# Kernel optimization log

Hardware: AMD Instinct MI355X
Metric: run time of the kernel (lower is better)

## Reference

```python
import jax, jax.numpy as jnp
import numpy as np

B, N = 16, 2048
NOTE, BEAT_H, MEAS_H, FINAL_H = 512, 128, 64, 128
NUM_BEATS, NUM_MEAS = 256, 64
OUT = 11            # output_size; QPM_INDEX = 0
QPM = 0


def _uniform(k, shape, fan):
    b = 1.0 / np.sqrt(fan)
    return jax.random.uniform(k, shape, jnp.float32, -b, b)


def _lstm_cell(x, h, c, wih, whh, bih, bhh):
    g = x @ wih.T + bih + h @ whh.T + bhh
    ii, ff, gg, oo = jnp.split(g, 4, axis=-1)
    c2 = jax.nn.sigmoid(ff) * c + jax.nn.sigmoid(ii) * jnp.tanh(gg)
    return jax.nn.sigmoid(oo) * jnp.tanh(c2), c2


def setup_inputs() -> dict:
    key = jax.random.key(0)
    ks = jax.random.split(key, 20)
    note_emb = jax.random.normal(ks[0], (B, N, NOTE), jnp.float32)
    beat_emb = jax.random.normal(ks[1], (B, NUM_BEATS, BEAT_H), jnp.float32)
    measure_emb = jax.random.normal(ks[2], (B, NUM_MEAS, MEAS_H), jnp.float32)
    beat_numbers = jnp.sort(jax.random.randint(ks[3], (B, N), 0, NUM_BEATS), axis=1)
    measure_numbers = beat_numbers // (NUM_BEATS // NUM_MEAS)
    tin = BEAT_H + MEAS_H + 1 + (OUT - 1)   # beat-tempo LSTM input size
    fin = NOTE + BEAT_H + MEAS_H + OUT      # final LSTM input size
    d = OUT - 1
    return {
        "note_emb": note_emb, "beat_emb": beat_emb, "measure_emb": measure_emb,
        "beat_numbers": beat_numbers, "measure_numbers": measure_numbers,
        "Wa": _uniform(ks[4], (d, d), d), "ba": _uniform(ks[5], (d,), d),
        "ctx": _uniform(ks[6], (d,), d),
        "Wih_t": _uniform(ks[7], (4 * BEAT_H, tin), BEAT_H),
        "Whh_t": _uniform(ks[8], (4 * BEAT_H, BEAT_H), BEAT_H),
        "bih_t": _uniform(ks[9], (4 * BEAT_H,), BEAT_H),
        "bhh_t": _uniform(ks[10], (4 * BEAT_H,), BEAT_H),
        "Wih_f": _uniform(ks[11], (4 * FINAL_H, fin), FINAL_H),
        "Whh_f": _uniform(ks[12], (4 * FINAL_H, FINAL_H), FINAL_H),
        "bih_f": _uniform(ks[13], (4 * FINAL_H,), FINAL_H),
        "bhh_f": _uniform(ks[14], (4 * FINAL_H,), FINAL_H),
        "W_fc": _uniform(ks[15], (d, FINAL_H), FINAL_H),
        "b_fc": _uniform(ks[16], (d,), FINAL_H),
        "W_tfc": _uniform(ks[17], (1, BEAT_H), BEAT_H),
        "b_tfc": _uniform(ks[18], (1,), BEAT_H),
    }


def _decode(note_emb, beat_emb, measure_emb, beat_numbers, measure_numbers,
            Wa, ba, ctx, Wih_t, Whh_t, bih_t, bhh_t,
            Wih_f, Whh_f, bih_f, bhh_f, W_fc, b_fc, W_tfc, b_tfc):
    Bn, Nn = note_emb.shape[0], note_emb.shape[1]
    d = W_fc.shape[0]  # OUT - 1
    zs_beat = jnp.maximum(beat_numbers - beat_numbers[:, :1], 0)
    zs_meas = jnp.maximum(measure_numbers - measure_numbers[:, :1], 0)
    diff = jnp.diff(beat_numbers, axis=1)
    # beat_changed: first step forced to 1, then diff of beat numbers
    changed_all = jnp.concatenate([jnp.ones((Bn, 1), diff.dtype), diff], axis=1) > 0
    pos = jnp.arange(Nn)
    bidx = jnp.arange(Bn)

    carry0 = (
        jnp.zeros((Bn, BEAT_H)), jnp.zeros((Bn, BEAT_H)),        # tempo h, c
        jnp.zeros((Bn, FINAL_H)), jnp.zeros((Bn, FINAL_H)),      # final h, c
        jnp.zeros((Bn, d + 1)),                                   # prev_out
        jnp.zeros((Bn, beat_emb.shape[1], d)),                    # beat_results
        jnp.zeros((Bn, Nn, d + 1)),                               # out_total
    )

    def step(carry, i):
        th, tc, fh, fc_, prev_out, beat_results, out_total = carry
        changed = changed_all[:, i]                                # [B] bool
        # --- get_beat_corresp_out: notes j < i in the beat just finished ---
        prev_beat = beat_numbers[:, jnp.maximum(i - 1, 0)]         # [B]
        note_mask = (beat_numbers == prev_beat[:, None]) & (pos[None, :] < i)
        x = out_total[:, :, QPM + 1:]                              # [B,N,d]
        sim = (x @ Wa.T + ba) @ ctx                                # [B,N]
        sim = jnp.where(note_mask, sim, -1e9)
        w = jax.nn.softmax(sim, axis=1)
        result_node = jnp.einsum('bn,bnd->bd', w, x)
        result_node = jnp.where(note_mask.any(axis=1)[:, None], result_node, 0.0)
        cb = zs_beat[:, i]
        cm = zs_meas[:, i]
        # scatter result_node into beat_results only for batches whose beat changed
        old = beat_results[bidx, cb]
        beat_results = beat_results.at[bidx, cb].set(
            jnp.where(changed[:, None], result_node, old))
        # --- beat tempo RNN step (only applied where changed) ---
        tempo_in = jnp.concatenate([
            beat_emb[bidx, cb], measure_emb[bidx, cm],
            prev_out[:, QPM:QPM + 1], beat_results[bidx, cb]], axis=-1)
        th2, tc2 = _lstm_cell(tempo_in, th, tc, Wih_t, Whh_t, bih_t, bhh_t)
        th = jnp.where(changed[:, None], th2, th)
        tc = jnp.where(changed[:, None], tc2, tc)
        tmp_tempo = th2 @ W_tfc.T + b_tfc                          # [B,1]
        prev_out = prev_out.at[:, QPM:QPM + 1].set(
            jnp.where(changed[:, None], tmp_tempo, prev_out[:, QPM:QPM + 1]))
        # --- final note-level LSTM step (all batches) ---
        fin_in = jnp.concatenate([
            note_emb[:, i], beat_emb[bidx, cb], measure_emb[bidx, cm], prev_out], axis=-1)
        fh, fc_ = _lstm_cell(fin_in, fh, fc_, Wih_f, Whh_f, bih_f, bhh_f)
        out = fh @ W_fc.T + b_fc                                   # [B,d]
        prev_out = jnp.concatenate([prev_out[:, :QPM + 1], out], axis=-1)
        out_total = out_total.at[:, i].set(prev_out)
        return (th, tc, fh, fc_, prev_out, beat_results, out_total), None

    carry, _ = jax.lax.scan(step, carry0, jnp.arange(Nn))
    out_total = carry[-1]
    # zero out padded notes (note embedding all-zero rows)
    pad = (note_emb.sum(-1) == 0)[:, :, None]
    return jnp.where(pad, 0.0, out_total)


def reference(note_emb, beat_emb, measure_emb, beat_numbers, measure_numbers,
              Wa, ba, ctx, Wih_t, Whh_t, bih_t, bhh_t,
              Wih_f, Whh_f, bih_f, bhh_f, W_fc, b_fc, W_tfc, b_tfc):
    return _decode(note_emb, beat_emb, measure_emb, beat_numbers, measure_numbers,
                   Wa, ba, ctx, Wih_t, Whh_t, bih_t, bhh_t,
                   Wih_f, Whh_f, bih_f, bhh_f, W_fc, b_fc, W_tfc, b_tfc)
```

## Files before the change

kernel.cpp:

```cpp
#include <hip/hip_runtime.h>
#include <cstdint>
#include <cstddef>

#define B_      16
#define N_      2048
#define NOTE_   512
#define BEAT_H_ 128
#define MEAS_H_ 64
#define NBEATS_ 256
#define NMEAS_  64
#define OUT_    11
#define D_      10
#define TSTRIDE 136

typedef float f32x4 __attribute__((ext_vector_type(4)));
typedef unsigned int u32x4 __attribute__((ext_vector_type(4)));
typedef _Float16 h2v __attribute__((ext_vector_type(2)));

__device__ __forceinline__ float fexp2_(float x) {
#if __has_builtin(__builtin_amdgcn_exp2f)
    return __builtin_amdgcn_exp2f(x);
#else
    return exp2f(x);
#endif
}
__device__ __forceinline__ float frcp_(float x) {
#if __has_builtin(__builtin_amdgcn_rcpf)
    return __builtin_amdgcn_rcpf(x);
#else
    return 1.0f / x;
#endif
}
__device__ __forceinline__ float sigm_(float x) {
    return frcp_(1.0f + fexp2_(-1.4426950408889634f * x));
}
__device__ __forceinline__ float tanh_(float x) {
    return 1.0f - 2.0f * frcp_(fexp2_(2.8853900817779268f * x) + 1.0f);
}

__device__ __forceinline__ float dot2f_(unsigned wu, unsigned hu, float c) {
    union { unsigned u; h2v h; } a, bb;
    a.u = wu; bb.u = hu;
#if __has_builtin(__builtin_amdgcn_fdot2)
    return __builtin_amdgcn_fdot2(a.h, bb.h, c, false);
#else
    return c + (float)a.h[0] * (float)bb.h[0] + (float)a.h[1] * (float)bb.h[1];
#endif
}

__device__ __align__(16) _Float16 g_whh_h16[512 * 128];
__device__ float g_bias_eff[512];
__device__ float g_wtail0[512];
__device__ __align__(16) _Float16 g_wht_h16[512 * TSTRIDE];

__global__ __launch_bounds__(256) void pad_k(const float* __restrict__ note,
                                             int* __restrict__ padf) {
    int wave = threadIdx.x >> 6, lane = threadIdx.x & 63;
    int r = blockIdx.x * 4 + wave;
    const float* row = note + ((size_t)r << 9);
    float s = 0.f;
#pragma unroll
    for (int u = 0; u < 8; ++u) s += row[lane + (u << 6)];
#pragma unroll
    for (int off = 32; off; off >>= 1) s += __shfl_xor(s, off, 64);
    if (lane == 0) padf[r] = (s == 0.0f) ? 1 : 0;
}

__global__ __launch_bounds__(128) void fold_whh(
    const float* __restrict__ Whh_f, const float* __restrict__ Wih_f,
    const float* __restrict__ W_fc, const float* __restrict__ b_fc) {
    int gr = blockIdx.x;
    int t = threadIdx.x;
    __shared__ float tail[OUT_];
    if (t < OUT_) tail[t] = Wih_f[(size_t)gr * 715 + 704 + t];
    __syncthreads();
    float m = Whh_f[(size_t)gr * 128 + t];
#pragma unroll
    for (int d = 0; d < D_; ++d) m += tail[1 + d] * W_fc[d * 128 + t];
    g_whh_h16[(size_t)gr * 128 + t] = (_Float16)m;
    if (t == 0) {
        float bb = 0.f;
#pragma unroll
        for (int d = 0; d < D_; ++d) bb += tail[1 + d] * b_fc[d];
        g_bias_eff[gr] = bb;
        g_wtail0[gr] = tail[0];
    }
}

__global__ __launch_bounds__(128) void fold_wht(const float* __restrict__ Whh_t) {
    int gr = blockIdx.x, t = threadIdx.x;
    g_wht_h16[(size_t)gr * TSTRIDE + t] = (_Float16)Whh_t[(size_t)gr * 128 + t];
    if (t < TSTRIDE - 128) g_wht_h16[(size_t)gr * TSTRIDE + 128 + t] = (_Float16)0.f;
}

__global__ __launch_bounds__(256) void tempo_pre_k(
    const float* __restrict__ beat, const float* __restrict__ meas,
    const int* __restrict__ bnum, const int* __restrict__ mnum,
    const float* __restrict__ Wih_t, const float* __restrict__ bih_t,
    const float* __restrict__ bhh_t, float* __restrict__ tpre) {
    __shared__ float sin_[16][192];
    int b = blockIdx.x, qt = blockIdx.y;
    int t = threadIdx.x;
    int bn0 = bnum[b << 11], mn0 = mnum[b << 11];
    for (int idx = t; idx < 16 * 192; idx += 256) {
        int qq = idx / 192, kk = idx - qq * 192;
        int q = qt * 16 + qq;
        float v;
        if (kk < 128) {
            v = beat[(size_t)(b * NBEATS_ + q) * 128 + kk];
        } else {
            int cm = ((q + bn0) >> 2) - mn0;
            if (cm > 63) cm = 63;
            if (cm < 0) cm = 0;
            v = meas[(size_t)(b * NMEAS_ + cm) * 64 + (kk - 128)];
        }
        sin_[qq][kk] = v;
    }
    __syncthreads();
    for (int half = 0; half < 2; ++half) {
        int j = t + half * 256;
        const float* wr = Wih_t + (size_t)j * 203;
        float bias = bih_t[j] + bhh_t[j];
        float acc[16] = {};
        for (int k = 0; k < 192; ++k) {
            float w = wr[k];
#pragma unroll
            for (int qq = 0; qq < 16; ++qq) acc[qq] += w * sin_[qq][k];
        }
        for (int qq = 0; qq < 16; ++qq)
            tpre[(size_t)(b * NBEATS_ + qt * 16 + qq) * 512 + j] = acc[qq] + bias;
    }
}

__global__ __launch_bounds__(256) void fin_pre_gemm(
    const float* __restrict__ note, const float* __restrict__ beat,
    const float* __restrict__ meas, const int* __restrict__ bnum,
    const int* __restrict__ mnum, const float* __restrict__ Wih_f,
    const float* __restrict__ bih_f, const float* __restrict__ bhh_f,
    float* __restrict__ finp) {
    __shared__ float As[16][64];
    __shared__ float Bs[16][64];
    int t = threadIdx.x;
    int r0 = blockIdx.x * 64;
    int j0 = blockIdx.y * 64;

    int am = t >> 2, alane = t & 3;
    int r = r0 + am;
    int b = r >> 11;
    int rb = b << 11;
    int cb = bnum[r] - bnum[rb];
    int cm = mnum[r] - mnum[rb];
    const float* arow_note = note + ((size_t)r << 9);
    const float* arow_beat = beat + ((size_t)(b * NBEATS_ + cb) << 7);
    const float* arow_meas = meas + ((size_t)(b * NMEAS_ + cm) << 6);

    int jj = t >> 2, blane = t & 3;
    const float* brow = Wih_f + (size_t)(j0 + jj) * 715;

    int tm0 = (t & 15) * 4, tn0 = (t >> 4) * 4;
    float acc[4][4] = {};

    for (int k0 = 0; k0 < 704; k0 += 16) {
        int ka = k0 + alane * 4;
        float4 av;
        if (ka < 512)      av = *(const float4*)(arow_note + ka);
        else if (ka < 640) av = *(const float4*)(arow_beat + (ka - 512));
        else               av = *(const float4*)(arow_meas + (ka - 640));
        int kb = k0 + blane * 4;
        float b0 = brow[kb], b1 = brow[kb + 1], b2 = brow[kb + 2], b3 = brow[kb + 3];
        __syncthreads();
        As[alane * 4 + 0][am] = av.x;
        As[alane * 4 + 1][am] = av.y;
        As[alane * 4 + 2][am] = av.z;
        As[alane * 4 + 3][am] = av.w;
        Bs[blane * 4 + 0][jj] = b0;
        Bs[blane * 4 + 1][jj] = b1;
        Bs[blane * 4 + 2][jj] = b2;
        Bs[blane * 4 + 3][jj] = b3;
        __syncthreads();
#pragma unroll
        for (int kk = 0; kk < 16; ++kk) {
            float4 a4 = *(const float4*)&As[kk][tm0];
            float4 b4 = *(const float4*)&Bs[kk][tn0];
            float aa[4] = {a4.x, a4.y, a4.z, a4.w};
            float bb[4] = {b4.x, b4.y, b4.z, b4.w};
#pragma unroll
            for (int mi = 0; mi < 4; ++mi)
#pragma unroll
                for (int ni = 0; ni < 4; ++ni) acc[mi][ni] += aa[mi] * bb[ni];
        }
    }
    float bias[4], beff[4];
#pragma unroll
    for (int ni = 0; ni < 4; ++ni) {
        int j = j0 + tn0 + ni;
        bias[ni] = bih_f[j] + bhh_f[j];
        beff[ni] = g_bias_eff[j];
    }
#pragma unroll
    for (int mi = 0; mi < 4; ++mi) {
        int rr = r0 + tm0 + mi;
        float eb = (rr & 2047) ? 1.0f : 0.0f;
        float4 o;
        o.x = acc[mi][0] + bias[0] + eb * beff[0];
        o.y = acc[mi][1] + bias[1] + eb * beff[1];
        o.z = acc[mi][2] + bias[2] + eb * beff[2];
        o.w = acc[mi][3] + bias[3] + eb * beff[3];
        *(float4*)(finp + ((size_t)rr << 9) + j0 + tn0) = o;
    }
}

__global__ __launch_bounds__(512)
__attribute__((amdgpu_waves_per_eu(2, 2)))
void decode_seq(
    float* finp,
    const float* __restrict__ tpre, const int* __restrict__ bnum,
    const float* __restrict__ Wih_t,
    const float* __restrict__ W_fc, const float* __restrict__ b_fc,
    const float* __restrict__ W_tfc, const float* __restrict__ b_tfc,
    const float* __restrict__ Wa, const float* __restrict__ ba,
    const float* __restrict__ ctx, float* __restrict__ tval) {
    __shared__ __align__(16) _Float16 wht16_s[512 * TSTRIDE];
    __shared__ __align__(16) _Float16 hf16_s[2][128];
    __shared__ __align__(16) _Float16 ht16_s[128];
    __shared__ __align__(16) _Float16 u16_s[128];
    __shared__ __align__(16) float hA_s[128];
    __shared__ __align__(16) float s_w_s[1024];
    __shared__ float wfcT[128][12];
    __shared__ float bfc_s[12];
    __shared__ float v_s[12];
    __shared__ float cur_res[12];
    __shared__ float pred_s[8];
    __shared__ float sc_s[4];
    __shared__ unsigned short run_start_s[300];
    __shared__ short run_cb_s[300];
    __shared__ int nruns_s;

    const int t = threadIdx.x, lane = t & 63, wave = t >> 6;
    const int b = blockIdx.x;
    const int bl = lane & 15;
    const int eidx = wave * 16 + bl;
    const int r_lane = (lane >> 4) * 128 + eidx;

    u32x4 wf0, wf1, wf2, wf3, wf4, wf5, wf6, wf7;
    u32x4 wf8, wf9, wf10, wf11, wf12, wf13, wf14, wf15;
    {
        const u32x4* wfp = (const u32x4*)(g_whh_h16 + (size_t)r_lane * 128);
        wf0 = wfp[0];   wf1 = wfp[1];   wf2 = wfp[2];   wf3 = wfp[3];
        wf4 = wfp[4];   wf5 = wfp[5];   wf6 = wfp[6];   wf7 = wfp[7];
        wf8 = wfp[8];   wf9 = wfp[9];   wf10 = wfp[10]; wf11 = wfp[11];
        wf12 = wfp[12]; wf13 = wfp[13]; wf14 = wfp[14]; wf15 = wfp[15];
    }
    asm volatile("" : "+v"(wf0), "+v"(wf1), "+v"(wf2), "+v"(wf3),
                      "+v"(wf4), "+v"(wf5), "+v"(wf6), "+v"(wf7));
    asm volatile("" : "+v"(wf8), "+v"(wf9), "+v"(wf10), "+v"(wf11),
                      "+v"(wf12), "+v"(wf13), "+v"(wf14), "+v"(wf15));

    const float wtail0_r = g_wtail0[r_lane];
    const float wtfc_r = W_tfc[eidx];
    float wiht_r[OUT_];
#pragma unroll
    for (int u = 0; u < OUT_; ++u) wiht_r[u] = Wih_t[(size_t)r_lane * 203 + 192 + u];

    {
        const uint4* src = (const uint4*)g_wht_h16;
        uint4* dst = (uint4*)wht16_s;
#pragma unroll
        for (int k = 0; k < 17; ++k) dst[t + 512 * k] = src[t + 512 * k];
    }
    for (int k = t; k < 128 * D_; k += 512) {
        int d = k >> 7, r = k & 127;
        wfcT[r][d] = W_fc[k];
    }
    if (t < 128) {
        hf16_s[0][t] = (_Float16)0.f;
        hf16_s[1][t] = (_Float16)0.f;
        ht16_s[t] = (_Float16)0.f;
    }
    if (t < D_) {
        bfc_s[t] = b_fc[t];
        cur_res[t] = 0.f;
        float vv = 0.f;
        for (int m = 0; m < D_; ++m) vv += ctx[m] * Wa[m * D_ + t];
        v_s[t] = vv;
    }
    if (t == 10) {
        float cc = 0.f;
        for (int m = 0; m < D_; ++m) cc += ba[m] * ctx[m];
        sc_s[0] = cc;
        sc_s[1] = b_tfc[0];
        sc_s[2] = 0.f;
    }
    const int* bnb = bnum + (b << 11);
    int bn0 = bnb[0];
    int base = t * 4;
    int bvm = (base == 0) ? 0 : bnb[base - 1];
    int bv0 = bnb[base], bv1 = bnb[base + 1], bv2 = bnb[base + 2], bv3 = bnb[base + 3];
    if (base == 0) bvm = bv0 - 1;
    int c = (bv0 != bvm) + (bv1 != bv0) + (bv2 != bv1) + (bv3 != bv2);
    ((int*)s_w_s)[t] = c;
    __syncthreads();
    if (t == 0) {
        float c1v = sc_s[0];
        for (int d = 0; d < D_; ++d) c1v += bfc_s[d] * v_s[d];
        sc_s[3] = c1v;
    }
    if (t < 128) {
        float uu = 0.f;
#pragma unroll
        for (int d = 0; d < D_; ++d) uu += v_s[d] * wfcT[t][d];
        u16_s[t] = (_Float16)uu;
    }
    if (wave == 0) {
        int c8[8], s = 0;
#pragma unroll
        for (int j = 0; j < 8; ++j) { c8[j] = ((int*)s_w_s)[lane * 8 + j]; s += c8[j]; }
        int incl = s;
#pragma unroll
        for (int off = 1; off < 64; off <<= 1) {
            int n = __shfl_up(incl, off, 64);
            if (lane >= off) incl += n;
        }
        int run = incl - s;
#pragma unroll
        for (int j = 0; j < 8; ++j) { ((int*)s_w_s)[512 + lane * 8 + j] = run; run += c8[j]; }
        if (lane == 63) nruns_s = incl;
    }
    __syncthreads();
    {
        int O = ((int*)s_w_s)[512 + t];
        if (bv0 != bvm) { run_start_s[O] = (unsigned short)(base + 0); run_cb_s[O] = (short)(bv0 - bn0); O++; }
        if (bv1 != bv0) { run_start_s[O] = (unsigned short)(base + 1); run_cb_s[O] = (short)(bv1 - bn0); O++; }
        if (bv2 != bv1) { run_start_s[O] = (unsigned short)(base + 2); run_cb_s[O] = (short)(bv2 - bn0); O++; }
        if (bv3 != bv2) { run_start_s[O] = (unsigned short)(base + 3); run_cb_s[O] = (short)(bv3 - bn0); O++; }
    }
    __syncthreads();
    const int nruns_r = nruns_s;

    char* hg = (char*)(finp + ((size_t)b << 11) * 512);
    const size_t fin_off = ((size_t)b << 11) * 512 + (size_t)r_lane;
    float gf_cur = finp[fin_off];
    float gt_pre = tpre[(size_t)(b * NBEATS_) * 512 + r_lane];
    int cur_run = -1, next_start = 0, run_s = 0, S_prev = 0;
    int pb = 0;
    float cf_r = 0.f, ct_r = 0.f;

    for (int i = 0; i < N_; ++i) {
        const bool changed = (i == next_start);
        if (changed) {
            ++cur_run;
            S_prev = run_s;
            run_s = i;
            next_start = (cur_run + 1 < nruns_r) ? (int)run_start_s[cur_run + 1] : (N_ * 2);
        }
        float prev0 = sc_s[2];
        float gf_nxt = finp[fin_off + (size_t)(i + 1) * 512];

        float acc;
        {
            const u32x4* hq = (const u32x4*)&hf16_s[pb][0];
            float a0 = 0.f, a1 = 0.f, a2 = 0.f, a3 = 0.f;
#define MSTEP(W, K)                                            \
            { u32x4 H = hq[K];                                 \
              a0 = dot2f_(W.x, H.x, a0);                       \
              a1 = dot2f_(W.y, H.y, a1);                       \
              a2 = dot2f_(W.z, H.z, a2);                       \
              a3 = dot2f_(W.w, H.w, a3); }
            MSTEP(wf0, 0)   MSTEP(wf1, 1)   MSTEP(wf2, 2)   MSTEP(wf3, 3)
            MSTEP(wf4, 4)   MSTEP(wf5, 5)   MSTEP(wf6, 6)   MSTEP(wf7, 7)
            MSTEP(wf8, 8)   MSTEP(wf9, 9)   MSTEP(wf10, 10) MSTEP(wf11, 11)
            MSTEP(wf12, 12) MSTEP(wf13, 13) MSTEP(wf14, 14) MSTEP(wf15, 15)
#undef MSTEP
            acc = (a0 + a1) + (a2 + a3);
        }
        float gmain = gf_cur + acc;
        gf_cur = gf_nxt;
        float tv = prev0;

        if (!changed) {
            float g = gmain + wtail0_r * prev0;
            float gF = __shfl(g, bl + 16, 64);
            float gG = __shfl(g, bl + 32, 64);
            float gO = __shfl(g, bl + 48, 64);
            if (lane < 16) {
                float c2 = sigm_(gF) * cf_r + sigm_(g) * tanh_(gG);
                float h2 = sigm_(gO) * tanh_(c2);
                cf_r = c2;
                hf16_s[pb ^ 1][eidx] = (_Float16)h2;
                *(_Float16*)(hg + (size_t)i * 2048 + (eidx << 1)) = (_Float16)h2;
            }
        } else {
            float gt;
            {
                const u32x4* wq = (const u32x4*)(wht16_s + (size_t)r_lane * TSTRIDE);
                const u32x4* hq = (const u32x4*)ht16_s;
                float a0 = 0.f, a1 = 0.f, a2 = 0.f, a3 = 0.f;
#pragma unroll
                for (int k = 0; k < 16; ++k) {
                    u32x4 W = wq[k];
                    u32x4 H = hq[k];
                    a0 = dot2f_(W.x, H.x, a0);
                    a1 = dot2f_(W.y, H.y, a1);
                    a2 = dot2f_(W.z, H.z, a2);
                    a3 = dot2f_(W.w, H.w, a3);
                }
                gt = gt_pre + (a0 + a1) + (a2 + a3) + wiht_r[0] * prev0;
            }
            if (cur_run + 1 < nruns_r)
                gt_pre = tpre[(size_t)(b * NBEATS_ + (int)run_cb_s[cur_run + 1]) * 512 + r_lane];

            if (wave == 0) {
                int Lc = i - S_prev;
                if (Lc > 1024) Lc = 1024;
                const char* hgB = hg + (size_t)S_prev * 2048;
                const float c1 = sc_s[3];
                float lmax = -1e30f;
                for (int j = lane; j < Lc; j += 64) {
                    const u32x4* hrow = (const u32x4*)(hgB + (size_t)j * 2048);
                    const u32x4* uq = (const u32x4*)u16_s;
                    float a0 = 0.f, a1 = 0.f, a2 = 0.f, a3 = 0.f;
#pragma unroll
                    for (int k = 0; k < 16; ++k) {
                        u32x4 hv = hrow[k], uv = uq[k];
                        a0 = dot2f_(hv.x, uv.x, a0);
                        a1 = dot2f_(hv.y, uv.y, a1);
                        a2 = dot2f_(hv.z, uv.z, a2);
                        a3 = dot2f_(hv.w, uv.w, a3);
                    }
                    float s = c1 + (a0 + a1) + (a2 + a3);
                    s_w_s[j] = s;
                    lmax = fmaxf(lmax, s);
                }
#pragma unroll
                for (int off = 32; off; off >>= 1)
                    lmax = fmaxf(lmax, __shfl_xor(lmax, off, 64));
                float lsum = 0.f;
                for (int j = lane; j < Lc; j += 64) {
                    float w = fexp2_(1.4426950408889634f * (s_w_s[j] - lmax));
                    s_w_s[j] = w;
                    lsum += w;
                }
#pragma unroll
                for (int off = 32; off; off >>= 1) lsum += __shfl_xor(lsum, off, 64);
                float inv = (Lc > 0) ? (1.0f / lsum) : 0.f;
                float hA0 = 0.f, hA1 = 0.f;
                for (int j = 0; j < Lc; ++j) {
                    unsigned hv = *(const unsigned*)(hgB + (size_t)j * 2048 + (lane << 2));
                    float w = s_w_s[j];
                    union { unsigned u; _Float16 h[2]; } hu; hu.u = hv;
                    hA0 += w * (float)hu.h[0];
                    hA1 += w * (float)hu.h[1];
                }
                hA_s[2 * lane] = hA0 * inv;
                hA_s[2 * lane + 1] = hA1 * inv;
                int dd = lane >> 3, rl = lane & 7, d2 = 8 + dd;
                float po1 = 0.f, po2 = 0.f;
                for (int k2 = 0; k2 < 16; ++k2) {
                    int r = rl + (k2 << 3);
                    float hv = hA_s[r];
                    po1 += hv * wfcT[r][dd];
                    if (d2 < D_) po2 += hv * wfcT[r][d2];
                }
                po1 += __shfl_xor(po1, 1, 64); po1 += __shfl_xor(po1, 2, 64); po1 += __shfl_xor(po1, 4, 64);
                po2 += __shfl_xor(po2, 1, 64); po2 += __shfl_xor(po2, 2, 64); po2 += __shfl_xor(po2, 4, 64);
                if (rl == 0) {
                    cur_res[dd] = (Lc > 0) ? (po1 + bfc_s[dd]) : 0.f;
                    if (d2 < D_) cur_res[d2] = (Lc > 0) ? (po2 + bfc_s[d2]) : 0.f;
                }
            }
            __syncthreads();
#pragma unroll
            for (int d = 0; d < D_; ++d) gt += wiht_r[1 + d] * cur_res[d];
            float gF = __shfl(gt, bl + 16, 64);
            float gG = __shfl(gt, bl + 32, 64);
            float gO = __shfl(gt, bl + 48, 64);
            if (lane < 16) {
                float c2 = sigm_(gF) * ct_r + sigm_(gt) * tanh_(gG);
                float h2 = sigm_(gO) * tanh_(c2);
                ct_r = c2;
                ht16_s[eidx] = (_Float16)h2;
                float p = h2 * wtfc_r;
                p += __shfl_xor(p, 1, 64);
                p += __shfl_xor(p, 2, 64);
                p += __shfl_xor(p, 4, 64);
                p += __shfl_xor(p, 8, 64);
                if (bl == 0) pred_s[wave] = p;
            }
            __syncthreads();
            float tnew = sc_s[1];
#pragma unroll
            for (int wv = 0; wv < 8; ++wv) tnew += pred_s[wv];
            tv = tnew;
            float g = gmain + wtail0_r * tnew;
            float gF2 = __shfl(g, bl + 16, 64);
            float gG2 = __shfl(g, bl + 32, 64);
            float gO2 = __shfl(g, bl + 48, 64);
            if (lane < 16) {
                float c2 = sigm_(gF2) * cf_r + sigm_(g) * tanh_(gG2);
                float h2 = sigm_(gO2) * tanh_(c2);
                cf_r = c2;
                hf16_s[pb ^ 1][eidx] = (_Float16)h2;
                *(_Float16*)(hg + (size_t)i * 2048 + (eidx << 1)) = (_Float16)h2;
            }
            if (t == 0) sc_s[2] = tnew;
        }
        if (t == 0) tval[(b << 11) + i] = tv;
        __syncthreads();
        pb ^= 1;
    }
}

__global__ __launch_bounds__(256) void out_k(
    const float* __restrict__ finp, const float* __restrict__ tval,
    const int* __restrict__ padf, const float* __restrict__ W_fc,
    const float* __restrict__ b_fc, float* __restrict__ out) {
    int g = blockIdx.x * 256 + threadIdx.x;
    int row = g >> 4, slot = g & 15;
    if (row >= B_ * N_) return;
    int pd = padf[row];
    float* orow = out + (size_t)row * OUT_;
    if (slot == 10) {
        orow[0] = pd ? 0.f : tval[row];
        return;
    }
    if (slot > 10) return;
    const unsigned* h2 = (const unsigned*)(finp + (size_t)row * 512);
    const float* wr = W_fc + slot * 128;
    float acc = b_fc[slot];
#pragma unroll 8
    for (int k = 0; k < 64; ++k) {
        union { unsigned u; _Float16 h[2]; } hv; hv.u = h2[k];
        acc += (float)hv.h[0] * wr[2 * k] + (float)hv.h[1] * wr[2 * k + 1];
    }
    orow[1 + slot] = pd ? 0.f : acc;
}

extern "C" void kernel_launch(void* const* d_in, const int* in_sizes, int n_in,
                              void* d_out, int out_size, void* d_ws, size_t ws_size,
                              hipStream_t stream) {
    const float* note  = (const float*)d_in[0];
    const float* beat  = (const float*)d_in[1];
    const float* meas  = (const float*)d_in[2];
    const int*   bnum  = (const int*)d_in[3];
    const int*   mnum  = (const int*)d_in[4];
    const float* Wa    = (const float*)d_in[5];
    const float* ba    = (const float*)d_in[6];
    const float* ctx   = (const float*)d_in[7];
    const float* Wih_t = (const float*)d_in[8];
    const float* Whh_t = (const float*)d_in[9];
    const float* bih_t = (const float*)d_in[10];
    const float* bhh_t = (const float*)d_in[11];
    const float* Wih_f = (const float*)d_in[12];
    const float* Whh_f = (const float*)d_in[13];
    const float* bih_f = (const float*)d_in[14];
    const float* bhh_f = (const float*)d_in[15];
    const float* W_fc  = (const float*)d_in[16];
    const float* b_fc  = (const float*)d_in[17];
    const float* W_tfc = (const float*)d_in[18];
    const float* b_tfc = (const float*)d_in[19];
    float* out = (float*)d_out;

    char* ws = (char*)d_ws;
    float* finp = (float*)ws;
    float* tpre = (float*)(ws + (size_t)64 * 1024 * 1024);
    int*   padf = (int*)(ws + (size_t)72 * 1024 * 1024);
    float* tval = (float*)(ws + (size_t)73 * 1024 * 1024);

    pad_k<<<8192, 256, 0, stream>>>(note, padf);
    fold_whh<<<512, 128, 0, stream>>>(Whh_f, Wih_f, W_fc, b_fc);
    fold_wht<<<512, 128, 0, stream>>>(Whh_t);
    tempo_pre_k<<<dim3(16, 16), 256, 0, stream>>>(beat, meas, bnum, mnum, Wih_t,
                                                  bih_t, bhh_t, tpre);
    fin_pre_gemm<<<dim3(512, 8), 256, 0, stream>>>(note, beat, meas, bnum, mnum,
                                                   Wih_f, bih_f, bhh_f, finp);
    decode_seq<<<16, 512, 0, stream>>>(finp, tpre, bnum, Wih_t,
                                       W_fc, b_fc, W_tfc, b_tfc, Wa, ba, ctx,
                                       tval);
    out_k<<<2048, 256, 0, stream>>>(finp, tval, padf, W_fc, b_fc, out);
}
```

Before: 3.879 ms.

## Halve decode block to 256 threads with interleaved gate layout and two rows per lane

The sequential decode kernel now runs with 256 threads instead of 512. Each lane computes two gate rows, one from the i/f pair and one from the g/o pair. The Whh weights are pre-permuted into an interleaved register/LDS layout, and the pre-GEMM outputs are column-permuted so each lane reads a float2. Gate exchange uses a single xor-32 shuffle, with tanh folded into a scaled sigmoid, and barriers become lighter lgkmcnt waits except at run boundaries. This aims to cut the per-step barrier and shuffle latency on the serial critical path. In exchange each lane holds 32 vector registers of weights and occupancy is one wave per EU.

```diff
diff --git a/kernel.cpp b/kernel.cpp
--- a/kernel.cpp
+++ b/kernel.cpp
@@ -11,7 +11,6 @@
 #define NMEAS_  64
 #define OUT_    11
 #define D_      10
-#define TSTRIDE 136
 
 typedef float f32x4 __attribute__((ext_vector_type(4)));
 typedef unsigned int u32x4 __attribute__((ext_vector_type(4)));
@@ -48,10 +47,16 @@
 #endif
 }
 
-__device__ __align__(16) _Float16 g_whh_h16[512 * 128];
+#define BAR_LDS() asm volatile("s_waitcnt lgkmcnt(0)\n\ts_barrier" ::: "memory")
+
+__device__ __forceinline__ void gstore16(void* p, _Float16 v) {
+    *(__attribute__((address_space(1))) _Float16*)p = v;
+}
+
+__device__ __align__(16) _Float16 g_w_i16[512 * 128];
 __device__ float g_bias_eff[512];
 __device__ float g_wtail0[512];
-__device__ __align__(16) _Float16 g_wht_h16[512 * TSTRIDE];
+__device__ __align__(16) _Float16 g_wht_i16[512 * 128];
 
 __global__ __launch_bounds__(256) void pad_k(const float* __restrict__ note,
                                              int* __restrict__ padf) {
@@ -77,7 +82,11 @@
     float m = Whh_f[(size_t)gr * 128 + t];
 #pragma unroll
     for (int d = 0; d < D_; ++d) m += tail[1 + d] * W_fc[d * 128 + t];
-    g_whh_h16[(size_t)gr * 128 + t] = (_Float16)m;
+    int g = gr >> 7, e = gr & 127;
+    int half = g >> 1, slot = g & 1;
+    int gl = ((e >> 5) << 6) + (e & 31) + (half << 5);
+    int k = slot * 16 + (t >> 3);
+    g_w_i16[(size_t)(k * 256 + gl) * 8 + (t & 7)] = (_Float16)m;
     if (t == 0) {
         float bb = 0.f;
 #pragma unroll
@@ -89,8 +98,11 @@
 
 __global__ __launch_bounds__(128) void fold_wht(const float* __restrict__ Whh_t) {
     int gr = blockIdx.x, t = threadIdx.x;
-    g_wht_h16[(size_t)gr * TSTRIDE + t] = (_Float16)Whh_t[(size_t)gr * 128 + t];
-    if (t < TSTRIDE - 128) g_wht_h16[(size_t)gr * TSTRIDE + 128 + t] = (_Float16)0.f;
+    int g = gr >> 7, e = gr & 127;
+    int half = g >> 1, slot = g & 1;
+    int gl = ((e >> 5) << 6) + (e & 31) + (half << 5);
+    int k = slot * 16 + (t >> 3);
+    g_wht_i16[(size_t)(k * 256 + gl) * 8 + (t & 7)] = (_Float16)Whh_t[(size_t)gr * 128 + t];
 }
 
 __global__ __launch_bounds__(256) void tempo_pre_k(
@@ -118,7 +130,8 @@
     }
     __syncthreads();
     for (int half = 0; half < 2; ++half) {
-        int j = t + half * 256;
+        int c = t + half * 256;
+        int j = ((c & 3) << 7) | (c >> 2);
         const float* wr = Wih_t + (size_t)j * 203;
         float bias = bih_t[j] + bhh_t[j];
         float acc[16] = {};
@@ -128,7 +141,7 @@
             for (int qq = 0; qq < 16; ++qq) acc[qq] += w * sin_[qq][k];
         }
         for (int qq = 0; qq < 16; ++qq)
-            tpre[(size_t)(b * NBEATS_ + qt * 16 + qq) * 512 + j] = acc[qq] + bias;
+            tpre[(size_t)(b * NBEATS_ + qt * 16 + qq) * 512 + c] = acc[qq] + bias;
     }
 }
 
@@ -155,7 +168,9 @@
     const float* arow_meas = meas + ((size_t)(b * NMEAS_ + cm) << 6);
 
     int jj = t >> 2, blane = t & 3;
-    const float* brow = Wih_f + (size_t)(j0 + jj) * 715;
+    int cB = j0 + jj;
+    int jB = ((cB & 3) << 7) | (cB >> 2);
+    const float* brow = Wih_f + (size_t)jB * 715;
 
     int tm0 = (t & 15) * 4, tn0 = (t >> 4) * 4;
     float acc[4][4] = {};
@@ -193,7 +208,8 @@
     float bias[4], beff[4];
 #pragma unroll
     for (int ni = 0; ni < 4; ++ni) {
-        int j = j0 + tn0 + ni;
+        int c = j0 + tn0 + ni;
+        int j = ((c & 3) << 7) | (c >> 2);
         bias[ni] = bih_f[j] + bhh_f[j];
         beff[ni] = g_bias_eff[j];
     }
@@ -210,8 +226,8 @@
     }
 }
 
-__global__ __launch_bounds__(512)
-__attribute__((amdgpu_waves_per_eu(2, 2)))
+__global__ __launch_bounds__(256)
+__attribute__((amdgpu_waves_per_eu(1, 1)))
 void decode_seq(
     float* finp,
     const float* __restrict__ tpre, const int* __restrict__ bnum,
@@ -220,8 +236,8 @@
     const float* __restrict__ W_tfc, const float* __restrict__ b_tfc,
     const float* __restrict__ Wa, const float* __restrict__ ba,
     const float* __restrict__ ctx, float* __restrict__ tval) {
-    __shared__ __align__(16) _Float16 wht16_s[512 * TSTRIDE];
-    __shared__ __align__(16) _Float16 hf16_s[2][128];
+    __shared__ __align__(16) u32x4 wht_i_s[32 * 256];
+    __shared__ __align__(16) _Float16 hbc16[2][128];
     __shared__ __align__(16) _Float16 ht16_s[128];
     __shared__ __align__(16) _Float16 u16_s[128];
     __shared__ __align__(16) float hA_s[128];
@@ -230,51 +246,66 @@
     __shared__ float bfc_s[12];
     __shared__ float v_s[12];
     __shared__ float cur_res[12];
-    __shared__ float pred_s[8];
+    __shared__ float pred_s[4];
     __shared__ float sc_s[4];
     __shared__ unsigned short run_start_s[300];
     __shared__ short run_cb_s[300];
     __shared__ int nruns_s;
 
-    const int t = threadIdx.x, lane = t & 63, wave = t >> 6;
+    const int t = threadIdx.x, l = t & 63, wid = t >> 6;
     const int b = blockIdx.x;
-    const int bl = lane & 15;
-    const int eidx = wave * 16 + bl;
-    const int r_lane = (lane >> 4) * 128 + eidx;
-
-    u32x4 wf0, wf1, wf2, wf3, wf4, wf5, wf6, wf7;
-    u32x4 wf8, wf9, wf10, wf11, wf12, wf13, wf14, wf15;
+    const int half = l >> 5;
+    const int e = wid * 32 + (l & 31);
+    const int rowA = (half * 2) * 128 + e;
+    const int rowB = (half * 2 + 1) * 128 + e;
+    const float kmul = half ? 2.0f : 1.0f;
+    const float badd = half ? -1.0f : 0.0f;
+
+    const float* finb = finp + ((size_t)b << 11) * 512;
+    char* hg = (char*)finb;
+    const int colByte = (e << 4) + (half << 3);
+
     {
-        const u32x4* wfp = (const u32x4*)(g_whh_h16 + (size_t)r_lane * 128);
-        wf0 = wfp[0];   wf1 = wfp[1];   wf2 = wfp[2];   wf3 = wfp[3];
-        wf4 = wfp[4];   wf5 = wfp[5];   wf6 = wfp[6];   wf7 = wfp[7];
-        wf8 = wfp[8];   wf9 = wfp[9];   wf10 = wfp[10]; wf11 = wfp[11];
-        wf12 = wfp[12]; wf13 = wfp[13]; wf14 = wfp[14]; wf15 = wfp[15];
-    }
-    asm volatile("" : "+v"(wf0), "+v"(wf1), "+v"(wf2), "+v"(wf3),
-                      "+v"(wf4), "+v"(wf5), "+v"(wf6), "+v"(wf7));
-    asm volatile("" : "+v"(wf8), "+v"(wf9), "+v"(wf10), "+v"(wf11),
-                      "+v"(wf12), "+v"(wf13), "+v"(wf14), "+v"(wf15));
-
-    const float wtail0_r = g_wtail0[r_lane];
-    const float wtfc_r = W_tfc[eidx];
-    float wiht_r[OUT_];
-#pragma unroll
-    for (int u = 0; u < OUT_; ++u) wiht_r[u] = Wih_t[(size_t)r_lane * 203 + 192 + u];
-
+        const u32x4* src = (const u32x4*)g_wht_i16;
+#pragma unroll
+        for (int k2 = 0; k2 < 32; ++k2) wht_i_s[k2 * 256 + t] = src[k2 * 256 + t];
+    }
+
+    u32x4 wreg[32];
     {
-        const uint4* src = (const uint4*)g_wht_h16;
-        uint4* dst = (uint4*)wht16_s;
-#pragma unroll
-        for (int k = 0; k < 17; ++k) dst[t + 512 * k] = src[t + 512 * k];
-    }
-    for (int k = t; k < 128 * D_; k += 512) {
+        const u32x4* gw = (const u32x4*)g_w_i16;
+#pragma unroll
+        for (int k = 0; k < 32; ++k) wreg[k] = gw[k * 256 + t];
+    }
+    asm volatile("" : "+v"(wreg[0]), "+v"(wreg[1]), "+v"(wreg[2]), "+v"(wreg[3]),
+                      "+v"(wreg[4]), "+v"(wreg[5]), "+v"(wreg[6]), "+v"(wreg[7]));
+    asm volatile("" : "+v"(wreg[8]), "+v"(wreg[9]), "+v"(wreg[10]), "+v"(wreg[11]),
+                      "+v"(wreg[12]), "+v"(wreg[13]), "+v"(wreg[14]), "+v"(wreg[15]));
+    asm volatile("" : "+v"(wreg[16]), "+v"(wreg[17]), "+v"(wreg[18]), "+v"(wreg[19]),
+                      "+v"(wreg[20]), "+v"(wreg[21]), "+v"(wreg[22]), "+v"(wreg[23]));
+    asm volatile("" : "+v"(wreg[24]), "+v"(wreg[25]), "+v"(wreg[26]), "+v"(wreg[27]),
+                      "+v"(wreg[28]), "+v"(wreg[29]), "+v"(wreg[30]), "+v"(wreg[31]));
+
+    const float wt0A = g_wtail0[rowA];
+    const float wt0B = g_wtail0[rowB];
+    const float wtfc_r = W_tfc[e];
+    const float btfc_r = b_tfc[0];
+    float wiht0A = Wih_t[(size_t)rowA * 203 + 192];
+    float wiht0B = Wih_t[(size_t)rowB * 203 + 192];
+    float wihtdA[D_], wihtdB[D_];
+#pragma unroll
+    for (int d = 0; d < D_; ++d) {
+        wihtdA[d] = Wih_t[(size_t)rowA * 203 + 193 + d];
+        wihtdB[d] = Wih_t[(size_t)rowB * 203 + 193 + d];
+    }
+
+    for (int k = t; k < 128 * D_; k += 256) {
         int d = k >> 7, r = k & 127;
         wfcT[r][d] = W_fc[k];
     }
     if (t < 128) {
-        hf16_s[0][t] = (_Float16)0.f;
-        hf16_s[1][t] = (_Float16)0.f;
+        hbc16[0][t] = (_Float16)0.f;
+        hbc16[1][t] = (_Float16)0.f;
         ht16_s[t] = (_Float16)0.f;
     }
     if (t < D_) {
@@ -288,16 +319,20 @@
         float cc = 0.f;
         for (int m = 0; m < D_; ++m) cc += ba[m] * ctx[m];
         sc_s[0] = cc;
-        sc_s[1] = b_tfc[0];
-        sc_s[2] = 0.f;
     }
     const int* bnb = bnum + (b << 11);
     int bn0 = bnb[0];
-    int base = t * 4;
-    int bvm = (base == 0) ? 0 : bnb[base - 1];
-    int bv0 = bnb[base], bv1 = bnb[base + 1], bv2 = bnb[base + 2], bv3 = bnb[base + 3];
-    if (base == 0) bvm = bv0 - 1;
-    int c = (bv0 != bvm) + (bv1 != bv0) + (bv2 != bv1) + (bv3 != bv2);
+    int base = t * 8;
+    int bv[8];
+#pragma unroll
+    for (int j = 0; j < 8; ++j) bv[j] = bnb[base + j];
+    int prevv = base ? bnb[base - 1] : (bv[0] - 1);
+    int c = 0;
+    {
+        int vv = prevv;
+#pragma unroll
+        for (int j = 0; j < 8; ++j) { c += (bv[j] != vv); vv = bv[j]; }
+    }
     ((int*)s_w_s)[t] = c;
     __syncthreads();
     if (t == 0) {
@@ -311,40 +346,43 @@
         for (int d = 0; d < D_; ++d) uu += v_s[d] * wfcT[t][d];
         u16_s[t] = (_Float16)uu;
     }
-    if (wave == 0) {
-        int c8[8], s = 0;
-#pragma unroll
-        for (int j = 0; j < 8; ++j) { c8[j] = ((int*)s_w_s)[lane * 8 + j]; s += c8[j]; }
-        int incl = s;
+    {
+        int incl = c;
 #pragma unroll
         for (int off = 1; off < 64; off <<= 1) {
             int n = __shfl_up(incl, off, 64);
-            if (lane >= off) incl += n;
-        }
-        int run = incl - s;
-#pragma unroll
-        for (int j = 0; j < 8; ++j) { ((int*)s_w_s)[512 + lane * 8 + j] = run; run += c8[j]; }
-        if (lane == 63) nruns_s = incl;
-    }
-    __syncthreads();
-    {
-        int O = ((int*)s_w_s)[512 + t];
-        if (bv0 != bvm) { run_start_s[O] = (unsigned short)(base + 0); run_cb_s[O] = (short)(bv0 - bn0); O++; }
-        if (bv1 != bv0) { run_start_s[O] = (unsigned short)(base + 1); run_cb_s[O] = (short)(bv1 - bn0); O++; }
-        if (bv2 != bv1) { run_start_s[O] = (unsigned short)(base + 2); run_cb_s[O] = (short)(bv2 - bn0); O++; }
-        if (bv3 != bv2) { run_start_s[O] = (unsigned short)(base + 3); run_cb_s[O] = (short)(bv3 - bn0); O++; }
+            if (l >= off) incl += n;
+        }
+        if (l == 63) ((int*)s_w_s)[512 + wid] = incl;
+        __syncthreads();
+        int woff = 0;
+        for (int w = 0; w < wid; ++w) woff += ((int*)s_w_s)[512 + w];
+        int O = woff + incl - c;
+        int vv = prevv;
+#pragma unroll
+        for (int j = 0; j < 8; ++j) {
+            if (bv[j] != vv) {
+                run_start_s[O] = (unsigned short)(base + j);
+                run_cb_s[O] = (short)(bv[j] - bn0);
+                O++;
+            }
+            vv = bv[j];
+        }
+        if (t == 0)
+            nruns_s = ((int*)s_w_s)[512] + ((int*)s_w_s)[513] +
+                      ((int*)s_w_s)[514] + ((int*)s_w_s)[515];
     }
     __syncthreads();
     const int nruns_r = nruns_s;
 
-    char* hg = (char*)(finp + ((size_t)b << 11) * 512);
-    const size_t fin_off = ((size_t)b << 11) * 512 + (size_t)r_lane;
-    float gf_cur = finp[fin_off];
-    float gt_pre = tpre[(size_t)(b * NBEATS_) * 512 + r_lane];
+    float2 gf_cur = *(const float2*)((const char*)finb + colByte);
+    float2 tp_cur = *(const float2*)((const char*)(tpre + (size_t)(b * NBEATS_) * 512) + colByte);
     int cur_run = -1, next_start = 0, run_s = 0, S_prev = 0;
     int pb = 0;
     float cf_r = 0.f, ct_r = 0.f;
-
+    float prev0_r = 0.f;
+
+#pragma unroll 1
     for (int i = 0; i < N_; ++i) {
         const bool changed = (i == next_start);
         if (changed) {
@@ -353,81 +391,81 @@
             run_s = i;
             next_start = (cur_run + 1 < nruns_r) ? (int)run_start_s[cur_run + 1] : (N_ * 2);
         }
-        float prev0 = sc_s[2];
-        float gf_nxt = finp[fin_off + (size_t)(i + 1) * 512];
-
-        float acc;
+        int inx = (i + 1 < N_) ? (i + 1) : i;
+        float2 gf_nxt = *(const float2*)((const char*)finb + (size_t)inx * 2048 + colByte);
+
+        float a0 = 0.f, a1 = 0.f, a2 = 0.f, a3 = 0.f;
+        float b0 = 0.f, b1 = 0.f, b2 = 0.f, b3 = 0.f;
         {
-            const u32x4* hq = (const u32x4*)&hf16_s[pb][0];
-            float a0 = 0.f, a1 = 0.f, a2 = 0.f, a3 = 0.f;
-#define MSTEP(W, K)                                            \
-            { u32x4 H = hq[K];                                 \
-              a0 = dot2f_(W.x, H.x, a0);                       \
-              a1 = dot2f_(W.y, H.y, a1);                       \
-              a2 = dot2f_(W.z, H.z, a2);                       \
-              a3 = dot2f_(W.w, H.w, a3); }
-            MSTEP(wf0, 0)   MSTEP(wf1, 1)   MSTEP(wf2, 2)   MSTEP(wf3, 3)
-            MSTEP(wf4, 4)   MSTEP(wf5, 5)   MSTEP(wf6, 6)   MSTEP(wf7, 7)
-            MSTEP(wf8, 8)   MSTEP(wf9, 9)   MSTEP(wf10, 10) MSTEP(wf11, 11)
-            MSTEP(wf12, 12) MSTEP(wf13, 13) MSTEP(wf14, 14) MSTEP(wf15, 15)
-#undef MSTEP
-            acc = (a0 + a1) + (a2 + a3);
-        }
-        float gmain = gf_cur + acc;
+            const u32x4* hq = (const u32x4*)&hbc16[pb][0];
+#pragma unroll
+            for (int k = 0; k < 16; ++k) {
+                u32x4 H = hq[k];
+                a0 = dot2f_(wreg[k].x, H.x, a0);
+                a1 = dot2f_(wreg[k].y, H.y, a1);
+                a2 = dot2f_(wreg[k].z, H.z, a2);
+                a3 = dot2f_(wreg[k].w, H.w, a3);
+                b0 = dot2f_(wreg[16 + k].x, H.x, b0);
+                b1 = dot2f_(wreg[16 + k].y, H.y, b1);
+                b2 = dot2f_(wreg[16 + k].z, H.z, b2);
+                b3 = dot2f_(wreg[16 + k].w, H.w, b3);
+            }
+        }
+        const float baseA = gf_cur.x + ((a0 + a1) + (a2 + a3));
+        const float baseB = gf_cur.y + ((b0 + b1) + (b2 + b3));
         gf_cur = gf_nxt;
-        float tv = prev0;
+        float gA, gB, tv;
 
         if (!changed) {
-            float g = gmain + wtail0_r * prev0;
-            float gF = __shfl(g, bl + 16, 64);
-            float gG = __shfl(g, bl + 32, 64);
-            float gO = __shfl(g, bl + 48, 64);
-            if (lane < 16) {
-                float c2 = sigm_(gF) * cf_r + sigm_(g) * tanh_(gG);
-                float h2 = sigm_(gO) * tanh_(c2);
-                cf_r = c2;
-                hf16_s[pb ^ 1][eidx] = (_Float16)h2;
-                *(_Float16*)(hg + (size_t)i * 2048 + (eidx << 1)) = (_Float16)h2;
-            }
+            gA = baseA + wt0A * prev0_r;
+            gB = baseB + wt0B * prev0_r;
+            tv = prev0_r;
         } else {
-            float gt;
+            float t0 = 0.f, t1 = 0.f, t2 = 0.f, t3 = 0.f;
+            float u0 = 0.f, u1 = 0.f, u2 = 0.f, u3 = 0.f;
             {
-                const u32x4* wq = (const u32x4*)(wht16_s + (size_t)r_lane * TSTRIDE);
-                const u32x4* hq = (const u32x4*)ht16_s;
-                float a0 = 0.f, a1 = 0.f, a2 = 0.f, a3 = 0.f;
+                const u32x4* htq = (const u32x4*)ht16_s;
 #pragma unroll
                 for (int k = 0; k < 16; ++k) {
-                    u32x4 W = wq[k];
-                    u32x4 H = hq[k];
-                    a0 = dot2f_(W.x, H.x, a0);
-                    a1 = dot2f_(W.y, H.y, a1);
-                    a2 = dot2f_(W.z, H.z, a2);
-                    a3 = dot2f_(W.w, H.w, a3);
+                    u32x4 HT = htq[k];
+                    u32x4 WA = wht_i_s[k * 256 + t];
+                    u32x4 WB = wht_i_s[(16 + k) * 256 + t];
+                    t0 = dot2f_(WA.x, HT.x, t0);
+                    t1 = dot2f_(WA.y, HT.y, t1);
+                    t2 = dot2f_(WA.z, HT.z, t2);
+                    t3 = dot2f_(WA.w, HT.w, t3);
+                    u0 = dot2f_(WB.x, HT.x, u0);
+                    u1 = dot2f_(WB.y, HT.y, u1);
+                    u2 = dot2f_(WB.z, HT.z, u2);
+                    u3 = dot2f_(WB.w, HT.w, u3);
                 }
-                gt = gt_pre + (a0 + a1) + (a2 + a3) + wiht_r[0] * prev0;
-            }
-            if (cur_run + 1 < nruns_r)
-                gt_pre = tpre[(size_t)(b * NBEATS_ + (int)run_cb_s[cur_run + 1]) * 512 + r_lane];
-
-            if (wave == 0) {
+            }
+            float gtA = tp_cur.x + ((t0 + t1) + (t2 + t3)) + wiht0A * prev0_r;
+            float gtB = tp_cur.y + ((u0 + u1) + (u2 + u3)) + wiht0B * prev0_r;
+            if (cur_run + 1 < nruns_r) {
+                int cb2 = (int)run_cb_s[cur_run + 1];
+                tp_cur = *(const float2*)((const char*)(tpre + (size_t)(b * NBEATS_ + cb2) * 512) + colByte);
+            }
+
+            if (wid == 0) {
                 int Lc = i - S_prev;
                 if (Lc > 1024) Lc = 1024;
                 const char* hgB = hg + (size_t)S_prev * 2048;
                 const float c1 = sc_s[3];
                 float lmax = -1e30f;
-                for (int j = lane; j < Lc; j += 64) {
+                for (int j = l; j < Lc; j += 64) {
                     const u32x4* hrow = (const u32x4*)(hgB + (size_t)j * 2048);
                     const u32x4* uq = (const u32x4*)u16_s;
-                    float a0 = 0.f, a1 = 0.f, a2 = 0.f, a3 = 0.f;
+                    float s0 = 0.f, s1 = 0.f, s2 = 0.f, s3 = 0.f;
 #pragma unroll
                     for (int k = 0; k < 16; ++k) {
                         u32x4 hv = hrow[k], uv = uq[k];
-                        a0 = dot2f_(hv.x, uv.x, a0);
-                        a1 = dot2f_(hv.y, uv.y, a1);
-                        a2 = dot2f_(hv.z, uv.z, a2);
-                        a3 = dot2f_(hv.w, uv.w, a3);
+                        s0 = dot2f_(hv.x, uv.x, s0);
+                        s1 = dot2f_(hv.y, uv.y, s1);
+                        s2 = dot2f_(hv.z, uv.z, s2);
+                        s3 = dot2f_(hv.w, uv.w, s3);
                     }
-                    float s = c1 + (a0 + a1) + (a2 + a3);
+                    float s = c1 + ((s0 + s1) + (s2 + s3));
                     s_w_s[j] = s;
                     lmax = fmaxf(lmax, s);
                 }
@@ -435,7 +473,7 @@
                 for (int off = 32; off; off >>= 1)
                     lmax = fmaxf(lmax, __shfl_xor(lmax, off, 64));
                 float lsum = 0.f;
-                for (int j = lane; j < Lc; j += 64) {
+                for (int j = l; j < Lc; j += 64) {
                     float w = fexp2_(1.4426950408889634f * (s_w_s[j] - lmax));
                     s_w_s[j] = w;
                     lsum += w;
@@ -445,15 +483,15 @@
                 float inv = (Lc > 0) ? (1.0f / lsum) : 0.f;
                 float hA0 = 0.f, hA1 = 0.f;
                 for (int j = 0; j < Lc; ++j) {
-                    unsigned hv = *(const unsigned*)(hgB + (size_t)j * 2048 + (lane << 2));
+                    unsigned hv = *(const unsigned*)(hgB + (size_t)j * 2048 + (l << 2));
                     float w = s_w_s[j];
                     union { unsigned u; _Float16 h[2]; } hu; hu.u = hv;
                     hA0 += w * (float)hu.h[0];
                     hA1 += w * (float)hu.h[1];
                 }
-                hA_s[2 * lane] = hA0 * inv;
-                hA_s[2 * lane + 1] = hA1 * inv;
-                int dd = lane >> 3, rl = lane & 7, d2 = 8 + dd;
+                hA_s[2 * l] = hA0 * inv;
+                hA_s[2 * l + 1] = hA1 * inv;
+                int dd = l >> 3, rl = l & 7, d2 = 8 + dd;
                 float po1 = 0.f, po2 = 0.f;
                 for (int k2 = 0; k2 < 16; ++k2) {
                     int r = rl + (k2 << 3);
@@ -468,44 +506,55 @@
                     if (d2 < D_) cur_res[d2] = (Lc > 0) ? (po2 + bfc_s[d2]) : 0.f;
                 }
             }
-            __syncthreads();
-#pragma unroll
-            for (int d = 0; d < D_; ++d) gt += wiht_r[1 + d] * cur_res[d];
-            float gF = __shfl(gt, bl + 16, 64);
-            float gG = __shfl(gt, bl + 32, 64);
-            float gO = __shfl(gt, bl + 48, 64);
-            if (lane < 16) {
-                float c2 = sigm_(gF) * ct_r + sigm_(gt) * tanh_(gG);
-                float h2 = sigm_(gO) * tanh_(c2);
+            BAR_LDS();
+#pragma unroll
+            for (int d = 0; d < D_; ++d) {
+                float cr = cur_res[d];
+                gtA += wihtdA[d] * cr;
+                gtB += wihtdB[d] * cr;
+            }
+            float actA = fmaf(kmul, sigm_(kmul * gtA), badd);
+            float actB = sigm_(gtB);
+            float shA = __shfl_xor(actA, 32, 64);
+            float shB = __shfl_xor(actB, 32, 64);
+            float p = 0.f;
+            if (l < 32) {
+                float c2 = actB * ct_r + actA * shA;
+                float h2 = shB * tanh_(c2);
                 ct_r = c2;
-                ht16_s[eidx] = (_Float16)h2;
-                float p = h2 * wtfc_r;
-                p += __shfl_xor(p, 1, 64);
-                p += __shfl_xor(p, 2, 64);
-                p += __shfl_xor(p, 4, 64);
-                p += __shfl_xor(p, 8, 64);
-                if (bl == 0) pred_s[wave] = p;
-            }
-            __syncthreads();
-            float tnew = sc_s[1];
-#pragma unroll
-            for (int wv = 0; wv < 8; ++wv) tnew += pred_s[wv];
+                ht16_s[e] = (_Float16)h2;
+                p = h2 * wtfc_r;
+            }
+            p += __shfl_xor(p, 1, 64);
+            p += __shfl_xor(p, 2, 64);
+            p += __shfl_xor(p, 4, 64);
+            p += __shfl_xor(p, 8, 64);
+            p += __shfl_xor(p, 16, 64);
+            if (l == 0) pred_s[wid] = p;
+            BAR_LDS();
+            float tnew = btfc_r + pred_s[0] + pred_s[1] + pred_s[2] + pred_s[3];
+            prev0_r = tnew;
             tv = tnew;
-            float g = gmain + wtail0_r * tnew;
-            float gF2 = __shfl(g, bl + 16, 64);
-            float gG2 = __shfl(g, bl + 32, 64);
-            float gO2 = __shfl(g, bl + 48, 64);
-            if (lane < 16) {
-                float c2 = sigm_(gF2) * cf_r + sigm_(g) * tanh_(gG2);
-                float h2 = sigm_(gO2) * tanh_(c2);
+            gA = baseA + wt0A * tnew;
+            gB = baseB + wt0B * tnew;
+        }
+
+        {
+            float actA = fmaf(kmul, sigm_(kmul * gA), badd);
+            float actB = sigm_(gB);
+            float shA = __shfl_xor(actA, 32, 64);
+            float shB = __shfl_xor(actB, 32, 64);
+            if (l < 32) {
+                float c2 = actB * cf_r + actA * shA;
+                float h2 = shB * tanh_(c2);
                 cf_r = c2;
-                hf16_s[pb ^ 1][eidx] = (_Float16)h2;
-                *(_Float16*)(hg + (size_t)i * 2048 + (eidx << 1)) = (_Float16)h2;
-            }
-            if (t == 0) sc_s[2] = tnew;
+                hbc16[pb ^ 1][e] = (_Float16)h2;
+                gstore16(hg + ((size_t)i << 11) + (e << 1), (_Float16)h2);
+            }
         }
         if (t == 0) tval[(b << 11) + i] = tv;
-        __syncthreads();
+        if (i + 1 == next_start) __syncthreads();
+        else BAR_LDS();
         pb ^= 1;
     }
 }
@@ -573,7 +622,7 @@
                                                   bih_t, bhh_t, tpre);
     fin_pre_gemm<<<dim3(512, 8), 256, 0, stream>>>(note, beat, meas, bnum, mnum,
                                                    Wih_f, bih_f, bhh_f, finp);
-    decode_seq<<<16, 512, 0, stream>>>(finp, tpre, bnum, Wih_t,
+    decode_seq<<<16, 256, 0, stream>>>(finp, tpre, bnum, Wih_t,
                                        W_fc, b_fc, W_tfc, b_tfc, Wa, ba, ctx,
                                        tval);
     out_k<<<2048, 256, 0, stream>>>(finp, tval, padf, W_fc, b_fc, out);
```

Measured after the change: 3.895 ms. About the same (+0.4%).
